# Kernel tuning notes

Hardware: AMD Instinct MI355X
Metric: run time of the kernel (lower is better)

Reference implementation:

```python
import jax, jax.numpy as jnp
import numpy as np

B, T, C, DK = 4096, 33, 512, 64  # batch, seq (== encoder_block_size), n_embd, d_k


def setup_inputs() -> dict:
    key = jax.random.key(0)
    k1, k2, k3, k4 = jax.random.split(key, 4)
    w_scale = 1.0 / np.sqrt(C).astype(np.float32)
    x = jax.random.normal(k1, (B, T, C), dtype=jnp.float32)
    Wq = jax.random.normal(k2, (DK, C), dtype=jnp.float32) * w_scale
    Wk = jax.random.normal(k3, (DK, C), dtype=jnp.float32) * w_scale
    Wv = jax.random.normal(k4, (DK, C), dtype=jnp.float32) * w_scale
    return {"x": x, "Wq": Wq, "Wk": Wk, "Wv": Wv}


def reference(x, Wq, Wk, Wv):
    # nn.Linear(n_embd, d_k, bias=False): y = x @ W.T
    q = jnp.einsum('btc,dc->btd', x, Wq)  # [B,T,DK]
    k = jnp.einsum('btc,dc->btd', x, Wk)
    v = jnp.einsum('btc,dc->btd', x, Wv)
    # NOTE: original scales by C**-0.5 (n_embd), not d_k**-0.5 — keep faithful.
    wei = jnp.einsum('btd,bsd->bts', q, k) * (C ** -0.5)  # [B,T,T]
    tril = jnp.tril(jnp.ones((T, T), dtype=bool))
    wei = jnp.where(tril, wei, -jnp.inf)
    wei = jax.nn.softmax(wei, axis=-1)
    # dropout p=0.0 -> identity
    out = jnp.einsum('bts,bsd->btd', wei, v)  # [B,T,DK]
    return out
```

## Files before the change

kernel.cpp:

```cpp
#include <hip/hip_runtime.h>
#include <hip/hip_bf16.h>


typedef __attribute__((ext_vector_type(8))) short bf16x8;
typedef __attribute__((ext_vector_type(4))) float floatx4;

#define NB 4096
#define TT 33
#define CC 512
#define DKK 64

#define XS 520
#define QS 72
#define VTS 72
#define SS 52
#define PS 72

__device__ __forceinline__ ushort f2b(float f) {
    union { __hip_bfloat16 h; ushort u; } cv;
    cv.h = __float2bfloat16(f);
    return cv.u;
}
__device__ __forceinline__ int imin(int a, int b) { return a < b ? a : b; }

__device__ __forceinline__ bf16x8 load8_b(const ushort* p) {
    return *(const bf16x8*)p;
}
__device__ __forceinline__ bf16x8 load8_f(const float* p) {
    float4 f0 = *(const float4*)p;
    float4 f1 = *(const float4*)(p + 4);
    bf16x8 r;
    r[0] = (short)f2b(f0.x); r[1] = (short)f2b(f0.y);
    r[2] = (short)f2b(f0.z); r[3] = (short)f2b(f0.w);
    r[4] = (short)f2b(f1.x); r[5] = (short)f2b(f1.y);
    r[6] = (short)f2b(f1.z); r[7] = (short)f2b(f1.w);
    return r;
}

__global__ void conv_w_kernel(const float* __restrict__ Wq,
                              const float* __restrict__ Wk,
                              const float* __restrict__ Wv,
                              ushort* __restrict__ wb) {
    const float* src = (blockIdx.y == 0) ? Wq : (blockIdx.y == 1) ? Wk : Wv;
    int i = (blockIdx.x * 256 + threadIdx.x) * 4;
    float4 f = *(const float4*)&src[i];
    ushort4 u;
    u.x = f2b(f.x); u.y = f2b(f.y); u.z = f2b(f.z); u.w = f2b(f.w);
    *(ushort4*)&wb[(size_t)blockIdx.y * 32768 + i] = u;
}

template <bool USE_WS>
__global__ __launch_bounds__(256, 2) void head_kernel(
    const float* __restrict__ x,
    const ushort* __restrict__ wb,
    const float* __restrict__ Wqf,
    const float* __restrict__ Wkf,
    const float* __restrict__ Wvf,
    float* __restrict__ out)
{
    __shared__ __align__(16) ushort x_s[TT * XS];
    __shared__ __align__(16) ushort q_s[TT * QS];
    __shared__ __align__(16) ushort k_s[TT * QS];
    __shared__ __align__(16) ushort vT_s[64 * VTS];
    __shared__ __align__(16) float  S_s[TT * SS];
    __shared__ __align__(16) ushort p_s[TT * PS];

    const int b    = blockIdx.x;
    const int tid  = threadIdx.x;
    const int lane = tid & 63;
    const int wave = tid >> 6;
    const int l15  = lane & 15;
    const int quad = lane >> 4;

    const uint4 z4 = make_uint4(0u, 0u, 0u, 0u);
    for (int i = tid; i < (64 * VTS) / 8; i += 256)
        ((uint4*)vT_s)[i] = z4;

    const float* xg = x + (size_t)b * (TT * CC);
    for (int i = tid; i < TT * 128; i += 256) {
        int r = i >> 7, c = (i & 127) << 2;
        float4 f = *(const float4*)&xg[r * CC + c];
        ushort4 u;
        u.x = f2b(f.x); u.y = f2b(f.y); u.z = f2b(f.z); u.w = f2b(f.w);
        *(ushort4*)&x_s[r * XS + c] = u;
    }
    __syncthreads();

    {
        floatx4 acc[3][3] = {};
        const ushort* wrow_b[3];
        const float*  wrow_f[3];
        int nidx[3];
        #pragma unroll
        for (int nl = 0; nl < 3; nl++) {
            int n = wave * 3 + nl;
            nidx[nl] = n;
            int mat = n >> 2;
            int row = (n & 3) * 16 + l15;
            if (USE_WS) {
                wrow_b[nl] = wb + (size_t)mat * 32768 + (size_t)row * CC;
                wrow_f[nl] = nullptr;
            } else {
                const float* Wf = (mat == 0) ? Wqf : (mat == 1) ? Wkf : Wvf;
                wrow_f[nl] = Wf + (size_t)row * CC;
                wrow_b[nl] = nullptr;
            }
        }
        const int r0 = l15, r1 = 16 + l15, r2 = 32;
        for (int ks = 0; ks < 16; ks++) {
            int c = ks * 32 + quad * 8;
            bf16x8 a0 = *(const bf16x8*)&x_s[r0 * XS + c];
            bf16x8 a1 = *(const bf16x8*)&x_s[r1 * XS + c];
            bf16x8 a2 = *(const bf16x8*)&x_s[r2 * XS + c];
            bf16x8 b0 = USE_WS ? load8_b(&wrow_b[0][c]) : load8_f(&wrow_f[0][c]);
            bf16x8 b1 = USE_WS ? load8_b(&wrow_b[1][c]) : load8_f(&wrow_f[1][c]);
            bf16x8 b2 = USE_WS ? load8_b(&wrow_b[2][c]) : load8_f(&wrow_f[2][c]);
            acc[0][0] = __builtin_amdgcn_mfma_f32_16x16x32_bf16(a0, b0, acc[0][0], 0, 0, 0);
            acc[1][0] = __builtin_amdgcn_mfma_f32_16x16x32_bf16(a1, b0, acc[1][0], 0, 0, 0);
            acc[2][0] = __builtin_amdgcn_mfma_f32_16x16x32_bf16(a2, b0, acc[2][0], 0, 0, 0);
            acc[0][1] = __builtin_amdgcn_mfma_f32_16x16x32_bf16(a0, b1, acc[0][1], 0, 0, 0);
            acc[1][1] = __builtin_amdgcn_mfma_f32_16x16x32_bf16(a1, b1, acc[1][1], 0, 0, 0);
            acc[2][1] = __builtin_amdgcn_mfma_f32_16x16x32_bf16(a2, b1, acc[2][1], 0, 0, 0);
            acc[0][2] = __builtin_amdgcn_mfma_f32_16x16x32_bf16(a0, b2, acc[0][2], 0, 0, 0);
            acc[1][2] = __builtin_amdgcn_mfma_f32_16x16x32_bf16(a1, b2, acc[1][2], 0, 0, 0);
            acc[2][2] = __builtin_amdgcn_mfma_f32_16x16x32_bf16(a2, b2, acc[2][2], 0, 0, 0);
        }
        #pragma unroll
        for (int nl = 0; nl < 3; nl++) {
            int n = nidx[nl];
            int mat = n >> 2;
            int col = (n & 3) * 16 + l15;
            #pragma unroll
            for (int m = 0; m < 3; m++) {
                #pragma unroll
                for (int r = 0; r < 4; r++) {
                    int row = m * 16 + quad * 4 + r;
                    if (row < TT) {
                        ushort v = f2b(acc[m][nl][r]);
                        if (mat == 0)      q_s[row * QS + col] = v;
                        else if (mat == 1) k_s[row * QS + col] = v;
                        else               vT_s[col * VTS + row] = v;
                    }
                }
            }
        }
    }
    __syncthreads();

    const float scale = 0.044194173824159216f;
    for (int g = wave; g < 9; g += 4) {
        int mt = g / 3, nt = g - mt * 3;
        floatx4 s = {};
        int ra = imin(mt * 16 + l15, 32);
        int rb = imin(nt * 16 + l15, 32);
        #pragma unroll
        for (int ks = 0; ks < 2; ks++) {
            int c = ks * 32 + quad * 8;
            bf16x8 aq = *(const bf16x8*)&q_s[ra * QS + c];
            bf16x8 bk = *(const bf16x8*)&k_s[rb * QS + c];
            s = __builtin_amdgcn_mfma_f32_16x16x32_bf16(aq, bk, s, 0, 0, 0);
        }
        #pragma unroll
        for (int r = 0; r < 4; r++) {
            int row = mt * 16 + quad * 4 + r;
            int col = nt * 16 + l15;
            if (row < TT) S_s[row * SS + col] = s[r] * scale;
        }
    }
    __syncthreads();

    if (tid < TT) {
        float* Sr = &S_s[tid * SS];
        float mx = -1e30f;
        for (int c = 0; c <= tid; c++) mx = fmaxf(mx, Sr[c]);
        float sum = 0.f;
        for (int c = 0; c <= tid; c++) { float e = __expf(Sr[c] - mx); Sr[c] = e; sum += e; }
        float inv = 1.f / sum;
        ushort* Pr = &p_s[tid * PS];
        int c = 0;
        for (; c <= tid; c++) Pr[c] = f2b(Sr[c] * inv);
        for (; c < 64; c++)  Pr[c] = 0;
    }
    __syncthreads();

    float* og = out + (size_t)b * (TT * DKK);
    for (int g = wave; g < 12; g += 4) {
        int mt = g >> 2, nt = g & 3;
        floatx4 o = {};
        int ra = imin(mt * 16 + l15, 32);
        int rb = nt * 16 + l15;
        #pragma unroll
        for (int ks = 0; ks < 2; ks++) {
            int c = ks * 32 + quad * 8;
            bf16x8 ap = *(const bf16x8*)&p_s[ra * PS + c];
            bf16x8 bv = *(const bf16x8*)&vT_s[rb * VTS + c];
            o = __builtin_amdgcn_mfma_f32_16x16x32_bf16(ap, bv, o, 0, 0, 0);
        }
        #pragma unroll
        for (int r = 0; r < 4; r++) {
            int t = mt * 16 + quad * 4 + r;
            if (t < TT) og[t * DKK + nt * 16 + l15] = o[r];
        }
    }
}

extern "C" void kernel_launch(void* const* d_in, const int* in_sizes, int n_in,
                              void* d_out, int out_size, void* d_ws, size_t ws_size,
                              hipStream_t stream) {
    const float* x  = (const float*)d_in[0];
    const float* Wq = (const float*)d_in[1];
    const float* Wk = (const float*)d_in[2];
    const float* Wv = (const float*)d_in[3];
    float* out = (float*)d_out;

    if (ws_size >= 3u * 64u * 512u * sizeof(ushort)) {
        ushort* wb = (ushort*)d_ws;
        conv_w_kernel<<<dim3(32, 3), 256, 0, stream>>>(Wq, Wk, Wv, wb);
        head_kernel<true><<<NB, 256, 0, stream>>>(x, wb, Wq, Wk, Wv, out);
    } else {
        head_kernel<false><<<NB, 256, 0, stream>>>(x, nullptr, Wq, Wk, Wv, out);
    }
}
```

Measured before the change: 519.5 us.

## Alias q/k/v/p/S shared buffers onto x tile to raise occupancy

Places the q, k, transposed v, probabilities and score buffers in one shared-memory arena that overlays the x staging tile. The tile is free once the projection MFMAs finish, which cuts shared memory per block to about 34 KB, and the launch bound rises from 2 to 4 blocks per CU. A barrier is added before the projection results are written back, the vT padding is zeroed after that point, and the softmax is unrolled with register-held rows and packed stores. The risk is higher register pressure from the unrolled softmax and the hoisted accumulators under the tighter launch bound.

```diff
diff --git a/kernel.cpp b/kernel.cpp
--- a/kernel.cpp
+++ b/kernel.cpp
@@ -8,13 +8,17 @@
 #define NB 4096
 #define TT 33
 #define CC 512
-#define DKK 64
-
-#define XS 520
-#define QS 72
-#define VTS 72
-#define SS 52
-#define PS 72
+
+#define XS   520
+#define QS   72
+#define SSTR 36
+
+#define OFF_Q   0
+#define OFF_K   4752
+#define OFF_VT  9504
+#define OFF_P   18720
+#define OFF_S   23472
+#define SMEM_BYTES 34320
 
 __device__ __forceinline__ ushort f2b(float f) {
     union { __hip_bfloat16 h; ushort u; } cv;
@@ -23,9 +27,7 @@
 }
 __device__ __forceinline__ int imin(int a, int b) { return a < b ? a : b; }
 
-__device__ __forceinline__ bf16x8 load8_b(const ushort* p) {
-    return *(const bf16x8*)p;
-}
+__device__ __forceinline__ bf16x8 load8_b(const ushort* p) { return *(const bf16x8*)p; }
 __device__ __forceinline__ bf16x8 load8_f(const float* p) {
     float4 f0 = *(const float4*)p;
     float4 f1 = *(const float4*)(p + 4);
@@ -50,7 +52,7 @@
 }
 
 template <bool USE_WS>
-__global__ __launch_bounds__(256, 2) void head_kernel(
+__global__ __launch_bounds__(256, 4) void head_kernel(
     const float* __restrict__ x,
     const ushort* __restrict__ wb,
     const float* __restrict__ Wqf,
@@ -58,12 +60,13 @@
     const float* __restrict__ Wvf,
     float* __restrict__ out)
 {
-    __shared__ __align__(16) ushort x_s[TT * XS];
-    __shared__ __align__(16) ushort q_s[TT * QS];
-    __shared__ __align__(16) ushort k_s[TT * QS];
-    __shared__ __align__(16) ushort vT_s[64 * VTS];
-    __shared__ __align__(16) float  S_s[TT * SS];
-    __shared__ __align__(16) ushort p_s[TT * PS];
+    __shared__ __align__(16) char smem[SMEM_BYTES];
+    ushort* x_s  = (ushort*)smem;
+    ushort* q_s  = (ushort*)(smem + OFF_Q);
+    ushort* k_s  = (ushort*)(smem + OFF_K);
+    ushort* vT_s = (ushort*)(smem + OFF_VT);
+    ushort* p_s  = (ushort*)(smem + OFF_P);
+    float*  S_s  = (float*)(smem + OFF_S);
 
     const int b    = blockIdx.x;
     const int tid  = threadIdx.x;
@@ -71,10 +74,6 @@
     const int wave = tid >> 6;
     const int l15  = lane & 15;
     const int quad = lane >> 4;
-
-    const uint4 z4 = make_uint4(0u, 0u, 0u, 0u);
-    for (int i = tid; i < (64 * VTS) / 8; i += 256)
-        ((uint4*)vT_s)[i] = z4;
 
     const float* xg = x + (size_t)b * (TT * CC);
     for (int i = tid; i < TT * 128; i += 256) {
@@ -86,26 +85,26 @@
     }
     __syncthreads();
 
+    floatx4 acc[3][3] = {};
+    int nidx[3];
+    const ushort* wrow_b[3];
+    const float*  wrow_f[3];
+    #pragma unroll
+    for (int nl = 0; nl < 3; nl++) {
+        int n = wave * 3 + nl;
+        nidx[nl] = n;
+        int mat = n >> 2;
+        int row = (n & 3) * 16 + l15;
+        if (USE_WS) {
+            wrow_b[nl] = wb + (size_t)mat * 32768 + (size_t)row * CC;
+            wrow_f[nl] = nullptr;
+        } else {
+            const float* Wf = (mat == 0) ? Wqf : (mat == 1) ? Wkf : Wvf;
+            wrow_f[nl] = Wf + (size_t)row * CC;
+            wrow_b[nl] = nullptr;
+        }
+    }
     {
-        floatx4 acc[3][3] = {};
-        const ushort* wrow_b[3];
-        const float*  wrow_f[3];
-        int nidx[3];
-        #pragma unroll
-        for (int nl = 0; nl < 3; nl++) {
-            int n = wave * 3 + nl;
-            nidx[nl] = n;
-            int mat = n >> 2;
-            int row = (n & 3) * 16 + l15;
-            if (USE_WS) {
-                wrow_b[nl] = wb + (size_t)mat * 32768 + (size_t)row * CC;
-                wrow_f[nl] = nullptr;
-            } else {
-                const float* Wf = (mat == 0) ? Wqf : (mat == 1) ? Wkf : Wvf;
-                wrow_f[nl] = Wf + (size_t)row * CC;
-                wrow_b[nl] = nullptr;
-            }
-        }
         const int r0 = l15, r1 = 16 + l15, r2 = 32;
         for (int ks = 0; ks < 16; ks++) {
             int c = ks * 32 + quad * 8;
@@ -125,22 +124,28 @@
             acc[1][2] = __builtin_amdgcn_mfma_f32_16x16x32_bf16(a1, b2, acc[1][2], 0, 0, 0);
             acc[2][2] = __builtin_amdgcn_mfma_f32_16x16x32_bf16(a2, b2, acc[2][2], 0, 0, 0);
         }
-        #pragma unroll
-        for (int nl = 0; nl < 3; nl++) {
-            int n = nidx[nl];
-            int mat = n >> 2;
-            int col = (n & 3) * 16 + l15;
+    }
+    __syncthreads();
+
+    for (int i = tid; i < 64 * 32; i += 256) {
+        int d = i >> 5, t = i & 31;
+        if (t) vT_s[d * QS + 32 + t] = 0;
+    }
+    #pragma unroll
+    for (int nl = 0; nl < 3; nl++) {
+        int n = nidx[nl];
+        int mat = n >> 2;
+        int col = (n & 3) * 16 + l15;
+        #pragma unroll
+        for (int m = 0; m < 3; m++) {
             #pragma unroll
-            for (int m = 0; m < 3; m++) {
-                #pragma unroll
-                for (int r = 0; r < 4; r++) {
-                    int row = m * 16 + quad * 4 + r;
-                    if (row < TT) {
-                        ushort v = f2b(acc[m][nl][r]);
-                        if (mat == 0)      q_s[row * QS + col] = v;
-                        else if (mat == 1) k_s[row * QS + col] = v;
-                        else               vT_s[col * VTS + row] = v;
-                    }
+            for (int r = 0; r < 4; r++) {
+                int row = m * 16 + quad * 4 + r;
+                if (row < TT) {
+                    ushort v = f2b(acc[m][nl][r]);
+                    if (mat == 0)      q_s[row * QS + col] = v;
+                    else if (mat == 1) k_s[row * QS + col] = v;
+                    else               vT_s[col * QS + row] = v;
                 }
             }
         }
@@ -164,26 +169,45 @@
         for (int r = 0; r < 4; r++) {
             int row = mt * 16 + quad * 4 + r;
             int col = nt * 16 + l15;
-            if (row < TT) S_s[row * SS + col] = s[r] * scale;
+            if (row < TT && col < TT) S_s[row * SSTR + col] = s[r] * scale;
         }
     }
     __syncthreads();
 
     if (tid < TT) {
-        float* Sr = &S_s[tid * SS];
+        const float* Sr = &S_s[tid * SSTR];
+        float4 f[9];
+        #pragma unroll
+        for (int j = 0; j < 9; j++) f[j] = *(const float4*)&Sr[4 * j];
+        const float* fv = (const float*)f;
         float mx = -1e30f;
-        for (int c = 0; c <= tid; c++) mx = fmaxf(mx, Sr[c]);
+        #pragma unroll
+        for (int c = 0; c < TT; c++)
+            mx = fmaxf(mx, (c <= tid) ? fv[c] : -1e30f);
+        float e[TT];
         float sum = 0.f;
-        for (int c = 0; c <= tid; c++) { float e = __expf(Sr[c] - mx); Sr[c] = e; sum += e; }
+        #pragma unroll
+        for (int c = 0; c < TT; c++) {
+            float t = __expf(fv[c] - mx);
+            e[c] = (c <= tid) ? t : 0.f;
+            sum += e[c];
+        }
         float inv = 1.f / sum;
-        ushort* Pr = &p_s[tid * PS];
-        int c = 0;
-        for (; c <= tid; c++) Pr[c] = f2b(Sr[c] * inv);
-        for (; c < 64; c++)  Pr[c] = 0;
-    }
-    __syncthreads();
-
-    float* og = out + (size_t)b * (TT * DKK);
+        ushort* Pr = &p_s[tid * QS];
+        #pragma unroll
+        for (int j = 0; j < 16; j++) {
+            uint pk = (uint)f2b(e[2 * j] * inv) | ((uint)f2b(e[2 * j + 1] * inv) << 16);
+            *(uint*)&Pr[2 * j] = pk;
+        }
+        Pr[32] = f2b(e[32] * inv);
+        Pr[33] = 0;
+        #pragma unroll
+        for (int j = 0; j < 15; j++)
+            *(uint*)&Pr[34 + 2 * j] = 0u;
+    }
+    __syncthreads();
+
+    float* og = out + (size_t)b * (TT * 64);
     for (int g = wave; g < 12; g += 4) {
         int mt = g >> 2, nt = g & 3;
         floatx4 o = {};
@@ -192,14 +216,14 @@
         #pragma unroll
         for (int ks = 0; ks < 2; ks++) {
             int c = ks * 32 + quad * 8;
-            bf16x8 ap = *(const bf16x8*)&p_s[ra * PS + c];
-            bf16x8 bv = *(const bf16x8*)&vT_s[rb * VTS + c];
+            bf16x8 ap = *(const bf16x8*)&p_s[ra * QS + c];
+            bf16x8 bv = *(const bf16x8*)&vT_s[rb * QS + c];
             o = __builtin_amdgcn_mfma_f32_16x16x32_bf16(ap, bv, o, 0, 0, 0);
         }
         #pragma unroll
         for (int r = 0; r < 4; r++) {
             int t = mt * 16 + quad * 4 + r;
-            if (t < TT) og[t * DKK + nt * 16 + l15] = o[r];
+            if (t < TT) og[t * 64 + nt * 16 + l15] = o[r];
         }
     }
 }
@@ -216,7 +240,7 @@
     if (ws_size >= 3u * 64u * 512u * sizeof(ushort)) {
         ushort* wb = (ushort*)d_ws;
         conv_w_kernel<<<dim3(32, 3), 256, 0, stream>>>(Wq, Wk, Wv, wb);
-        head_kernel<true><<<NB, 256, 0, stream>>>(x, wb, Wq, Wk, Wv, out);
+        head_kernel<true><<<NB, 256, 0, stream>>>(x, wb, nullptr, nullptr, nullptr, out);
     } else {
         head_kernel<false><<<NB, 256, 0, stream>>>(x, nullptr, Wq, Wk, Wv, out);
     }
```

Measured after the change: 463.3 us. -10.8%, faster.
